# Performance work log

Measured on AMD Instinct MI355X. Metric: run time of the kernel, lower is better.

Reference implementation:

```python
import math
import jax, jax.numpy as jnp
import numpy as np

B, S, D = 4, 2048, 1280
H, HD = 16, 80  # num_heads, head_dim
LOG2E = 1.442695041


def setup_inputs() -> dict:
    key = jax.random.key(0)
    ks = jax.random.split(key, 6)
    hidden_states = jax.random.normal(ks[0], (B, S, D), dtype=jnp.float32)
    # additive causal mask: 0 on/below diagonal, large negative above
    causal = jnp.tril(jnp.ones((S, S), dtype=bool))
    attention_mask = jnp.where(causal, 0.0, -1e9).astype(jnp.float32)[None, None, :, :]
    attention_mask = jnp.broadcast_to(attention_mask, (B, 1, S, S))
    scaling = jax.random.normal(ks[1], (HD,), dtype=jnp.float32)
    fan = 1.0 / math.sqrt(D)
    qkv_w = jax.random.normal(ks[2], (3 * H * HD, D), dtype=jnp.float32) * fan
    qkv_b = jax.random.normal(ks[3], (3 * H * HD,), dtype=jnp.float32) * fan
    o_w = jax.random.normal(ks[4], (D, H * HD), dtype=jnp.float32) * (1.0 / math.sqrt(H * HD))
    o_b = jax.random.normal(ks[5], (D,), dtype=jnp.float32) * fan
    return {
        "hidden_states": hidden_states,
        "attention_mask": attention_mask,
        "scaling": scaling,
        "qkv_w": qkv_w,
        "qkv_b": qkv_b,
        "o_w": o_w,
        "o_b": o_b,
    }


def reference(hidden_states, attention_mask, scaling, qkv_w, qkv_b, o_w, o_b):
    b, s, _ = hidden_states.shape
    qkv = hidden_states @ qkv_w.T + qkv_b  # [b, s, 3*H*HD]
    xq, xk, xv = jnp.split(qkv, [H * HD, 2 * H * HD], axis=-1)
    xq = xq.reshape(b, s, H, HD)
    xk = xk.reshape(b, s, H, HD)
    xv = xv.reshape(b, s, H, HD)
    # per-dim query scaling: softplus(scaling) * log2(e) / sqrt(head_dim)
    scale = jax.nn.softplus(scaling) * (LOG2E / math.sqrt(HD))
    xq = xq * scale[None, None, None, :]
    scores = jnp.einsum("bqhd,bkhd->bhqk", xq, xk) + attention_mask  # [b,H,s,s]
    probs = jax.nn.softmax(scores.astype(jnp.float32), axis=-1).astype(xq.dtype)
    out = jnp.einsum("bhqk,bkhd->bqhd", probs, xv).reshape(b, s, H * HD)
    return out @ o_w.T + o_b
```

## Files before the change

kernel.cpp:

```cpp
#include <hip/hip_runtime.h>
#include <math.h>

#define B_ 4
#define S_ 2048
#define D_ 1280
#define H_ 16
#define HD_ 80
#define HHD (H_ * HD_)
#define QKVN (3 * H_ * HD_)

typedef __bf16 bf16x8 __attribute__((ext_vector_type(8)));
typedef __bf16 bf16x4 __attribute__((ext_vector_type(4)));
typedef float  f32x4  __attribute__((ext_vector_type(4)));

__global__ __launch_bounds__(256) void cvt_bf16(
    const float* __restrict__ in, __bf16* __restrict__ out, int n8)
{
    const int i = blockIdx.x * 256 + threadIdx.x;
    if (i < n8) {
        const float4 a = ((const float4*)in)[2 * (size_t)i];
        const float4 b = ((const float4*)in)[2 * (size_t)i + 1];
        bf16x8 v = {(__bf16)a.x, (__bf16)a.y, (__bf16)a.z, (__bf16)a.w,
                    (__bf16)b.x, (__bf16)b.y, (__bf16)b.z, (__bf16)b.w};
        *(bf16x8*)(out + 8 * (size_t)i) = v;
    }
}

__device__ __forceinline__ void async_copy16(const void* g, void* l)
{
    __builtin_amdgcn_global_load_lds(
        (const __attribute__((address_space(1))) unsigned int*)g,
        (__attribute__((address_space(3))) unsigned int*)l, 16, 0, 0);
}

__device__ __forceinline__ void stage128x64(
    const __bf16* __restrict__ src, int K, char* lds, int tid)
{
    const int wave = tid >> 6, lane = tid & 63;
#pragma unroll
    for (int i = 0; i < 4; ++i) {
        const int c = (wave * 4 + i) * 64 + lane;
        const int r = c >> 3;
        const int g = (c & 7) ^ (r & 7);
        async_copy16(src + (size_t)r * K + g * 8, lds + (wave * 4 + i) * 1024);
    }
}

__device__ __forceinline__ bf16x8 frag_ld(const char* lds, int m, int j)
{
    return *(const bf16x8*)(lds + m * 128 + ((j ^ (m & 7)) << 4));
}

__device__ __forceinline__ void mfma_loop(
    const __bf16* __restrict__ A, const __bf16* __restrict__ W, int K,
    char* ldsA, char* ldsB, int tid, f32x4 acc[4][4])
{
    const int wave = tid >> 6;
    const int wm = wave >> 1, wn = wave & 1;
    const int l16 = tid & 15, quad = (tid & 63) >> 4;

#pragma unroll
    for (int mi = 0; mi < 4; ++mi)
#pragma unroll
        for (int ni = 0; ni < 4; ++ni) acc[mi][ni] = (f32x4){0.f, 0.f, 0.f, 0.f};

    for (int k0 = 0; k0 < K; k0 += 64) {
        __syncthreads();
        stage128x64(A + k0, K, ldsA, tid);
        stage128x64(W + k0, K, ldsB, tid);
        __syncthreads();
#pragma unroll
        for (int ks = 0; ks < 2; ++ks) {
            bf16x8 af[4], bfr[4];
#pragma unroll
            for (int mi = 0; mi < 4; ++mi)
                af[mi] = frag_ld(ldsA, wm * 64 + mi * 16 + l16, ks * 4 + quad);
#pragma unroll
            for (int ni = 0; ni < 4; ++ni)
                bfr[ni] = frag_ld(ldsB, wn * 64 + ni * 16 + l16, ks * 4 + quad);
#pragma unroll
            for (int mi = 0; mi < 4; ++mi)
#pragma unroll
                for (int ni = 0; ni < 4; ++ni)
                    acc[mi][ni] = __builtin_amdgcn_mfma_f32_16x16x32_bf16(
                        af[mi], bfr[ni], acc[mi][ni], 0, 0, 0);
        }
    }
}

__global__ __launch_bounds__(256) void gemm_qkv_mfma(
    const __bf16* __restrict__ Ab, const __bf16* __restrict__ Wb,
    const float* __restrict__ bias, const float* __restrict__ scaling,
    __bf16* __restrict__ Qb, __bf16* __restrict__ Kb, __bf16* __restrict__ Vtb)
{
    __shared__ __align__(16) char ldsA[128 * 128];
    __shared__ __align__(16) char ldsB[128 * 128];
    const int tid = threadIdx.x;
    const int m0 = blockIdx.y * 128, n0 = blockIdx.x * 128;

    f32x4 acc[4][4];
    mfma_loop(Ab + (size_t)m0 * D_, Wb + (size_t)n0 * D_, D_, ldsA, ldsB, tid, acc);

    const int wave = tid >> 6, wm = wave >> 1, wn = wave & 1;
    const int l16 = tid & 15, quad = (tid & 63) >> 4;
    const int sec = n0 / HHD;

#pragma unroll
    for (int ni = 0; ni < 4; ++ni) {
        const int col = n0 + wn * 64 + ni * 16 + l16;
        const int cis = col - sec * HHD;
        const int h = cis / HD_;
        const int d = cis - h * HD_;
        const float bv = bias[col];
        float qsv = 0.f;
        if (sec == 0)
            qsv = log1pf(expf(scaling[d])) *
                  (1.442695041f * 1.442695041f / 8.944271910f);
#pragma unroll
        for (int mi = 0; mi < 4; ++mi) {
#pragma unroll
            for (int r = 0; r < 4; ++r) {
                const int row = m0 + wm * 64 + mi * 16 + quad * 4 + r;
                const int bb = row >> 11;
                const int s = row & (S_ - 1);
                const size_t bh = (size_t)(bb * H_ + h);
                const float v = acc[mi][ni][r] + bv;
                if (sec == 0)      Qb[(bh * S_ + s) * HD_ + d] = (__bf16)(v * qsv);
                else if (sec == 1) Kb[(bh * S_ + s) * HD_ + d] = (__bf16)v;
                else               Vtb[(bh * HD_ + d) * S_ + s] = (__bf16)v;
            }
        }
    }
}

__global__ __launch_bounds__(256) void gemm_o_mfma(
    const __bf16* __restrict__ Ab, const __bf16* __restrict__ Wb,
    const float* __restrict__ bias, float* __restrict__ C)
{
    __shared__ __align__(16) char ldsA[128 * 128];
    __shared__ __align__(16) char ldsB[128 * 128];
    const int tid = threadIdx.x;
    const int m0 = blockIdx.y * 128, n0 = blockIdx.x * 128;

    f32x4 acc[4][4];
    mfma_loop(Ab + (size_t)m0 * D_, Wb + (size_t)n0 * D_, D_, ldsA, ldsB, tid, acc);

    const int wave = tid >> 6, wm = wave >> 1, wn = wave & 1;
    const int l16 = tid & 15, quad = (tid & 63) >> 4;

#pragma unroll
    for (int ni = 0; ni < 4; ++ni) {
        const int col = n0 + wn * 64 + ni * 16 + l16;
        const float bv = bias[col];
#pragma unroll
        for (int mi = 0; mi < 4; ++mi) {
#pragma unroll
            for (int r = 0; r < 4; ++r) {
                const int row = m0 + wm * 64 + mi * 16 + quad * 4 + r;
                C[(size_t)row * D_ + col] = acc[mi][ni][r] + bv;
            }
        }
    }
}

__global__ __launch_bounds__(256, 4) void attn_v7(
    const __bf16* __restrict__ Qb, const __bf16* __restrict__ Kb,
    const __bf16* __restrict__ Vtb, __bf16* __restrict__ out)
{
    __shared__ __align__(16) __bf16 Ps[4][2][16][40];

    const int tid = threadIdx.x;
    const int wave = tid >> 6;
    const int lane = tid & 63;
    const int l16 = lane & 15;
    const int quad = lane >> 4;
    const int b = blockIdx.z, h = blockIdx.y;
    const int bh = b * H_ + h;
    const int x = blockIdx.x;
    const int q_lo = 64 * x + 16 * wave;
    const int q_hi = 64 * (31 - x) + 16 * wave;

    const __bf16* Kbase = Kb + (size_t)bh * S_ * HD_;
    const __bf16* Vbase = Vtb + (size_t)bh * HD_ * S_;

    bf16x8 qfL[3], qfH[3];
    {
        const __bf16* QrowL = Qb + ((size_t)bh * S_ + q_lo + l16) * HD_;
        const __bf16* QrowH = Qb + ((size_t)bh * S_ + q_hi + l16) * HD_;
        qfL[0] = *(const bf16x8*)(QrowL + quad * 8);
        qfL[1] = *(const bf16x8*)(QrowL + 32 + quad * 8);
        qfH[0] = *(const bf16x8*)(QrowH + quad * 8);
        qfH[1] = *(const bf16x8*)(QrowH + 32 + quad * 8);
        bf16x8 zL = {}, zH = {};
        if (quad < 2) {
            zL = *(const bf16x8*)(QrowL + 64 + quad * 8);
            zH = *(const bf16x8*)(QrowH + 64 + quad * 8);
        }
        qfL[2] = zL; qfH[2] = zH;
    }

    float mL = -1e30f, lL = 0.f, mH = -1e30f, lH = 0.f;
    f32x4 oL[5], oH[5];
#pragma unroll
    for (int t = 0; t < 5; ++t) { oL[t] = (f32x4){0.f,0.f,0.f,0.f}; oH[t] = (f32x4){0.f,0.f,0.f,0.f}; }

    const int nkt_lo = (q_lo + 16 + 31) >> 5;
    const int nkt_hi = (q_hi + 16 + 31) >> 5;

    for (int kt = 0; kt < nkt_hi; ++kt) {
        const int k0 = kt * 32;
        const bool do_lo = (kt < nkt_lo);

        f32x4 sH[2], sL[2];
#pragma unroll
        for (int t = 0; t < 2; ++t) {
            const __bf16* Krow = Kbase + (size_t)(k0 + t * 16 + l16) * HD_;
            const bf16x8 kf0 = *(const bf16x8*)(Krow + quad * 8);
            const bf16x8 kf1 = *(const bf16x8*)(Krow + 32 + quad * 8);
            bf16x8 kf2 = {};
            if (quad < 2) kf2 = *(const bf16x8*)(Krow + 64 + quad * 8);

            f32x4 a = (f32x4){0.f,0.f,0.f,0.f};
            a = __builtin_amdgcn_mfma_f32_16x16x32_bf16(kf0, qfH[0], a, 0, 0, 0);
            a = __builtin_amdgcn_mfma_f32_16x16x32_bf16(kf1, qfH[1], a, 0, 0, 0);
            a = __builtin_amdgcn_mfma_f32_16x16x32_bf16(kf2, qfH[2], a, 0, 0, 0);
            sH[t] = a;
            if (do_lo) {
                f32x4 c = (f32x4){0.f,0.f,0.f,0.f};
                c = __builtin_amdgcn_mfma_f32_16x16x32_bf16(kf0, qfL[0], c, 0, 0, 0);
                c = __builtin_amdgcn_mfma_f32_16x16x32_bf16(kf1, qfL[1], c, 0, 0, 0);
                c = __builtin_amdgcn_mfma_f32_16x16x32_bf16(kf2, qfL[2], c, 0, 0, 0);
                sL[t] = c;
            }
        }

        float aH;
        {
            if (k0 + 31 > q_hi) {
#pragma unroll
                for (int t = 0; t < 2; ++t)
#pragma unroll
                    for (int i = 0; i < 4; ++i)
                        sH[t][i] = (k0 + t * 16 + quad * 4 + i <= q_hi + l16)
                                   ? sH[t][i] : -1e30f;
            }
            float mx = sH[0][0];
#pragma unroll
            for (int i = 1; i < 4; ++i) mx = fmaxf(mx, sH[0][i]);
#pragma unroll
            for (int i = 0; i < 4; ++i) mx = fmaxf(mx, sH[1][i]);
            mx = fmaxf(mx, __shfl_xor(mx, 16));
            mx = fmaxf(mx, __shfl_xor(mx, 32));
            const float mn = fmaxf(mH, mx);
            aH = exp2f(mH - mn);
            mH = mn;
            float rs = 0.f;
#pragma unroll
            for (int t = 0; t < 2; ++t)
#pragma unroll
                for (int i = 0; i < 4; ++i) {
                    const float p = exp2f(sH[t][i] - mn);
                    sH[t][i] = p;
                    rs += p;
                }
            rs += __shfl_xor(rs, 16);
            rs += __shfl_xor(rs, 32);
            lH = lH * aH + rs;
#pragma unroll
            for (int t = 0; t < 2; ++t) {
                bf16x4 pk = {(__bf16)sH[t][0], (__bf16)sH[t][1],
                             (__bf16)sH[t][2], (__bf16)sH[t][3]};
                *(bf16x4*)&Ps[wave][0][l16][t * 16 + quad * 4] = pk;
            }
        }

        float aL = 1.f;
        if (do_lo) {
            if (k0 + 31 > q_lo) {
#pragma unroll
                for (int t = 0; t < 2; ++t)
#pragma unroll
                    for (int i = 0; i < 4; ++i)
                        sL[t][i] = (k0 + t * 16 + quad * 4 + i <= q_lo + l16)
                                   ? sL[t][i] : -1e30f;
            }
            float mx = sL[0][0];
#pragma unroll
            for (int i = 1; i < 4; ++i) mx = fmaxf(mx, sL[0][i]);
#pragma unroll
            for (int i = 0; i < 4; ++i) mx = fmaxf(mx, sL[1][i]);
            mx = fmaxf(mx, __shfl_xor(mx, 16));
            mx = fmaxf(mx, __shfl_xor(mx, 32));
            const float mn = fmaxf(mL, mx);
            aL = exp2f(mL - mn);
            mL = mn;
            float rs = 0.f;
#pragma unroll
            for (int t = 0; t < 2; ++t)
#pragma unroll
                for (int i = 0; i < 4; ++i) {
                    const float p = exp2f(sL[t][i] - mn);
                    sL[t][i] = p;
                    rs += p;
                }
            rs += __shfl_xor(rs, 16);
            rs += __shfl_xor(rs, 32);
            lL = lL * aL + rs;
#pragma unroll
            for (int t = 0; t < 2; ++t) {
                bf16x4 pk = {(__bf16)sL[t][0], (__bf16)sL[t][1],
                             (__bf16)sL[t][2], (__bf16)sL[t][3]};
                *(bf16x4*)&Ps[wave][1][l16][t * 16 + quad * 4] = pk;
            }
        }

        bf16x8 vf[5];
#pragma unroll
        for (int t = 0; t < 5; ++t)
            vf[t] = *(const bf16x8*)(Vbase + (size_t)(t * 16 + l16) * S_ + k0 + quad * 8);

        asm volatile("s_waitcnt lgkmcnt(0)" ::: "memory");
        const bf16x8 pfH = *(const bf16x8*)&Ps[wave][0][l16][quad * 8];
        const bf16x8 pfL = *(const bf16x8*)&Ps[wave][1][l16][quad * 8];

#pragma unroll
        for (int t = 0; t < 5; ++t) {
            f32x4 c;
#pragma unroll
            for (int i = 0; i < 4; ++i) c[i] = oH[t][i] * aH;
            oH[t] = __builtin_amdgcn_mfma_f32_16x16x32_bf16(vf[t], pfH, c, 0, 0, 0);
            if (do_lo) {
                f32x4 d;
#pragma unroll
                for (int i = 0; i < 4; ++i) d[i] = oL[t][i] * aL;
                oL[t] = __builtin_amdgcn_mfma_f32_16x16x32_bf16(vf[t], pfL, d, 0, 0, 0);
            }
        }
    }

    const float invH = 1.f / lH;
    const float invL = 1.f / lL;
    const size_t rowH = ((size_t)b * S_ + q_hi + l16) * HHD + h * HD_ + quad * 4;
    const size_t rowL = ((size_t)b * S_ + q_lo + l16) * HHD + h * HD_ + quad * 4;
#pragma unroll
    for (int t = 0; t < 5; ++t) {
        bf16x4 ovH = {(__bf16)(oH[t][0] * invH), (__bf16)(oH[t][1] * invH),
                      (__bf16)(oH[t][2] * invH), (__bf16)(oH[t][3] * invH)};
        bf16x4 ovL = {(__bf16)(oL[t][0] * invL), (__bf16)(oL[t][1] * invL),
                      (__bf16)(oL[t][2] * invL), (__bf16)(oL[t][3] * invL)};
        *(bf16x4*)(out + rowH + t * 16) = ovH;
        *(bf16x4*)(out + rowL + t * 16) = ovL;
    }
}

extern "C" void kernel_launch(void* const* d_in, const int* in_sizes, int n_in,
                              void* d_out, int out_size, void* d_ws, size_t ws_size,
                              hipStream_t stream)
{
    const float* hidden  = (const float*)d_in[0];
    const float* scaling = (const float*)d_in[2];
    const float* qkv_w   = (const float*)d_in[3];
    const float* qkv_b   = (const float*)d_in[4];
    const float* o_w     = (const float*)d_in[5];
    const float* o_b     = (const float*)d_in[6];
    float* out = (float*)d_out;

    const size_t N_HID = (size_t)B_ * S_ * D_;
    const size_t N_QW  = (size_t)QKVN * D_;
    const size_t N_OW  = (size_t)D_ * D_;
    const size_t NPH   = (size_t)B_ * H_ * S_ * HD_;

    __bf16* Ab    = (__bf16*)d_ws;
    __bf16* Wqb   = Ab + N_HID;
    __bf16* Wob   = Wqb + N_QW;
    __bf16* Qb    = Wob + N_OW;
    __bf16* Kb    = Qb + NPH;
    __bf16* Vtb   = Kb + NPH;
    __bf16* attnb = Vtb + NPH;

    dim3 blk(256);

    cvt_bf16<<<dim3(N_HID / 8 / 256), blk, 0, stream>>>(hidden, Ab, N_HID / 8);
    cvt_bf16<<<dim3(N_QW  / 8 / 256), blk, 0, stream>>>(qkv_w, Wqb, N_QW / 8);
    cvt_bf16<<<dim3(N_OW  / 8 / 256), blk, 0, stream>>>(o_w,   Wob, N_OW / 8);

    gemm_qkv_mfma<<<dim3(QKVN / 128, B_ * S_ / 128), blk, 0, stream>>>(
        Ab, Wqb, qkv_b, scaling, Qb, Kb, Vtb);

    attn_v7<<<dim3(16, H_, B_), blk, 0, stream>>>(Qb, Kb, Vtb, attnb);

    gemm_o_mfma<<<dim3(D_ / 128, B_ * S_ / 128), blk, 0, stream>>>(
        attnb, Wob, o_b, out);
}
```

Before: 539.7 us.

## Double-buffer K fragments, remap attention grid, and defer row-sum reduction

The attention kernel now prefetches the next K tile into registers while the current tile is processed, using a ping-pong pair of register buffers. The V loads are issued at the top of each iteration so their global latency overlaps with the QK MFMAs, and s_setprio raises wave priority around the MFMA blocks. The row-sum shuffle reduction is moved out of the loop and done once at the end, which is valid because the per-lane partial sums share the same rescale factors. The grid is flattened and remapped so that 8 consecutive blocks come from different heads with the same x, which changes L2 locality and load balance. The cost is higher register pressure at 4 waves/SIMD occupancy.

After: 1.006 ms. 1.86x slower.

```diff
diff --git a/kernel.cpp b/kernel.cpp
--- a/kernel.cpp
+++ b/kernel.cpp
@@ -163,7 +163,20 @@
     }
 }
 
-__global__ __launch_bounds__(256, 4) void attn_v7(
+struct KF8 { bf16x8 f0, f1, f2; };
+
+__device__ __forceinline__ void kload8(
+    const __bf16* __restrict__ base, int row, int quad, KF8& kf)
+{
+    const __bf16* r = base + (size_t)row * HD_;
+    kf.f0 = *(const bf16x8*)(r + quad * 8);
+    kf.f1 = *(const bf16x8*)(r + 32 + quad * 8);
+    bf16x8 z = {};
+    if (quad < 2) z = *(const bf16x8*)(r + 64 + quad * 8);
+    kf.f2 = z;
+}
+
+__global__ __launch_bounds__(256, 4) void attn_v9(
     const __bf16* __restrict__ Qb, const __bf16* __restrict__ Kb,
     const __bf16* __restrict__ Vtb, __bf16* __restrict__ out)
 {
@@ -174,30 +187,23 @@
     const int lane = tid & 63;
     const int l16 = lane & 15;
     const int quad = lane >> 4;
-    const int b = blockIdx.z, h = blockIdx.y;
-    const int bh = b * H_ + h;
-    const int x = blockIdx.x;
+
+    const int flat = blockIdx.x;
+    const int slot = flat >> 3;
+    const int bh   = ((slot >> 4) << 3) + (flat & 7);
+    const int x    = slot & 15;
+    const int b = bh >> 4, h = bh & 15;
+
     const int q_lo = 64 * x + 16 * wave;
     const int q_hi = 64 * (31 - x) + 16 * wave;
 
+    const __bf16* Qbase = Qb + (size_t)bh * S_ * HD_;
     const __bf16* Kbase = Kb + (size_t)bh * S_ * HD_;
     const __bf16* Vbase = Vtb + (size_t)bh * HD_ * S_;
 
-    bf16x8 qfL[3], qfH[3];
-    {
-        const __bf16* QrowL = Qb + ((size_t)bh * S_ + q_lo + l16) * HD_;
-        const __bf16* QrowH = Qb + ((size_t)bh * S_ + q_hi + l16) * HD_;
-        qfL[0] = *(const bf16x8*)(QrowL + quad * 8);
-        qfL[1] = *(const bf16x8*)(QrowL + 32 + quad * 8);
-        qfH[0] = *(const bf16x8*)(QrowH + quad * 8);
-        qfH[1] = *(const bf16x8*)(QrowH + 32 + quad * 8);
-        bf16x8 zL = {}, zH = {};
-        if (quad < 2) {
-            zL = *(const bf16x8*)(QrowL + 64 + quad * 8);
-            zH = *(const bf16x8*)(QrowH + 64 + quad * 8);
-        }
-        qfL[2] = zL; qfH[2] = zH;
-    }
+    KF8 qL, qH;
+    kload8(Qbase, q_lo + l16, quad, qL);
+    kload8(Qbase, q_hi + l16, quad, qH);
 
     float mL = -1e30f, lL = 0.f, mH = -1e30f, lH = 0.f;
     f32x4 oL[5], oH[5];
@@ -207,31 +213,42 @@
     const int nkt_lo = (q_lo + 16 + 31) >> 5;
     const int nkt_hi = (q_hi + 16 + 31) >> 5;
 
-    for (int kt = 0; kt < nkt_hi; ++kt) {
+    KF8 kA[2], kB[2];
+    kload8(Kbase, l16, quad, kA[0]);
+    kload8(Kbase, 16 + l16, quad, kA[1]);
+
+    auto body = [&](int kt, KF8 (&cur)[2], KF8 (&nxt)[2]) {
         const int k0 = kt * 32;
         const bool do_lo = (kt < nkt_lo);
 
+        bf16x8 vf[5];
+#pragma unroll
+        for (int t = 0; t < 5; ++t)
+            vf[t] = *(const bf16x8*)(Vbase + (size_t)(t * 16 + l16) * S_ + k0 + quad * 8);
+
         f32x4 sH[2], sL[2];
+        __builtin_amdgcn_s_setprio(1);
 #pragma unroll
         for (int t = 0; t < 2; ++t) {
-            const __bf16* Krow = Kbase + (size_t)(k0 + t * 16 + l16) * HD_;
-            const bf16x8 kf0 = *(const bf16x8*)(Krow + quad * 8);
-            const bf16x8 kf1 = *(const bf16x8*)(Krow + 32 + quad * 8);
-            bf16x8 kf2 = {};
-            if (quad < 2) kf2 = *(const bf16x8*)(Krow + 64 + quad * 8);
-
             f32x4 a = (f32x4){0.f,0.f,0.f,0.f};
-            a = __builtin_amdgcn_mfma_f32_16x16x32_bf16(kf0, qfH[0], a, 0, 0, 0);
-            a = __builtin_amdgcn_mfma_f32_16x16x32_bf16(kf1, qfH[1], a, 0, 0, 0);
-            a = __builtin_amdgcn_mfma_f32_16x16x32_bf16(kf2, qfH[2], a, 0, 0, 0);
+            a = __builtin_amdgcn_mfma_f32_16x16x32_bf16(cur[t].f0, qH.f0, a, 0, 0, 0);
+            a = __builtin_amdgcn_mfma_f32_16x16x32_bf16(cur[t].f1, qH.f1, a, 0, 0, 0);
+            a = __builtin_amdgcn_mfma_f32_16x16x32_bf16(cur[t].f2, qH.f2, a, 0, 0, 0);
             sH[t] = a;
             if (do_lo) {
                 f32x4 c = (f32x4){0.f,0.f,0.f,0.f};
-                c = __builtin_amdgcn_mfma_f32_16x16x32_bf16(kf0, qfL[0], c, 0, 0, 0);
-                c = __builtin_amdgcn_mfma_f32_16x16x32_bf16(kf1, qfL[1], c, 0, 0, 0);
-                c = __builtin_amdgcn_mfma_f32_16x16x32_bf16(kf2, qfL[2], c, 0, 0, 0);
+                c = __builtin_amdgcn_mfma_f32_16x16x32_bf16(cur[t].f0, qL.f0, c, 0, 0, 0);
+                c = __builtin_amdgcn_mfma_f32_16x16x32_bf16(cur[t].f1, qL.f1, c, 0, 0, 0);
+                c = __builtin_amdgcn_mfma_f32_16x16x32_bf16(cur[t].f2, qL.f2, c, 0, 0, 0);
                 sL[t] = c;
             }
+        }
+        __builtin_amdgcn_s_setprio(0);
+
+        {
+            const int kn = (kt + 1 < nkt_hi ? kt + 1 : kt) * 32;
+            kload8(Kbase, kn + l16, quad, nxt[0]);
+            kload8(Kbase, kn + 16 + l16, quad, nxt[1]);
         }
 
         float aH;
@@ -244,11 +261,11 @@
                         sH[t][i] = (k0 + t * 16 + quad * 4 + i <= q_hi + l16)
                                    ? sH[t][i] : -1e30f;
             }
-            float mx = sH[0][0];
-#pragma unroll
-            for (int i = 1; i < 4; ++i) mx = fmaxf(mx, sH[0][i]);
-#pragma unroll
-            for (int i = 0; i < 4; ++i) mx = fmaxf(mx, sH[1][i]);
+            float m01 = fmaxf(sH[0][0], sH[0][1]);
+            float m23 = fmaxf(sH[0][2], sH[0][3]);
+            float m45 = fmaxf(sH[1][0], sH[1][1]);
+            float m67 = fmaxf(sH[1][2], sH[1][3]);
+            float mx = fmaxf(fmaxf(m01, m23), fmaxf(m45, m67));
             mx = fmaxf(mx, __shfl_xor(mx, 16));
             mx = fmaxf(mx, __shfl_xor(mx, 32));
             const float mn = fmaxf(mH, mx);
@@ -263,8 +280,6 @@
                     sH[t][i] = p;
                     rs += p;
                 }
-            rs += __shfl_xor(rs, 16);
-            rs += __shfl_xor(rs, 32);
             lH = lH * aH + rs;
 #pragma unroll
             for (int t = 0; t < 2; ++t) {
@@ -284,11 +299,11 @@
                         sL[t][i] = (k0 + t * 16 + quad * 4 + i <= q_lo + l16)
                                    ? sL[t][i] : -1e30f;
             }
-            float mx = sL[0][0];
-#pragma unroll
-            for (int i = 1; i < 4; ++i) mx = fmaxf(mx, sL[0][i]);
-#pragma unroll
-            for (int i = 0; i < 4; ++i) mx = fmaxf(mx, sL[1][i]);
+            float m01 = fmaxf(sL[0][0], sL[0][1]);
+            float m23 = fmaxf(sL[0][2], sL[0][3]);
+            float m45 = fmaxf(sL[1][0], sL[1][1]);
+            float m67 = fmaxf(sL[1][2], sL[1][3]);
+            float mx = fmaxf(fmaxf(m01, m23), fmaxf(m45, m67));
             mx = fmaxf(mx, __shfl_xor(mx, 16));
             mx = fmaxf(mx, __shfl_xor(mx, 32));
             const float mn = fmaxf(mL, mx);
@@ -303,8 +318,6 @@
                     sL[t][i] = p;
                     rs += p;
                 }
-            rs += __shfl_xor(rs, 16);
-            rs += __shfl_xor(rs, 32);
             lL = lL * aL + rs;
 #pragma unroll
             for (int t = 0; t < 2; ++t) {
@@ -314,15 +327,11 @@
             }
         }
 
-        bf16x8 vf[5];
-#pragma unroll
-        for (int t = 0; t < 5; ++t)
-            vf[t] = *(const bf16x8*)(Vbase + (size_t)(t * 16 + l16) * S_ + k0 + quad * 8);
-
         asm volatile("s_waitcnt lgkmcnt(0)" ::: "memory");
         const bf16x8 pfH = *(const bf16x8*)&Ps[wave][0][l16][quad * 8];
         const bf16x8 pfL = *(const bf16x8*)&Ps[wave][1][l16][quad * 8];
 
+        __builtin_amdgcn_s_setprio(1);
 #pragma unroll
         for (int t = 0; t < 5; ++t) {
             f32x4 c;
@@ -336,10 +345,23 @@
                 oL[t] = __builtin_amdgcn_mfma_f32_16x16x32_bf16(vf[t], pfL, d, 0, 0, 0);
             }
         }
-    }
-
-    const float invH = 1.f / lH;
-    const float invL = 1.f / lL;
+        __builtin_amdgcn_s_setprio(0);
+    };
+
+    int kt = 0;
+    while (true) {
+        body(kt, kA, kB);
+        if (++kt == nkt_hi) break;
+        body(kt, kB, kA);
+        if (++kt == nkt_hi) break;
+    }
+
+    float lHs = lH + __shfl_xor(lH, 16);
+    lHs += __shfl_xor(lHs, 32);
+    float lLs = lL + __shfl_xor(lL, 16);
+    lLs += __shfl_xor(lLs, 32);
+    const float invH = 1.f / lHs;
+    const float invL = 1.f / lLs;
     const size_t rowH = ((size_t)b * S_ + q_hi + l16) * HHD + h * HD_ + quad * 4;
     const size_t rowL = ((size_t)b * S_ + q_lo + l16) * HHD + h * HD_ + quad * 4;
 #pragma unroll
@@ -387,7 +409,7 @@
     gemm_qkv_mfma<<<dim3(QKVN / 128, B_ * S_ / 128), blk, 0, stream>>>(
         Ab, Wqb, qkv_b, scaling, Qb, Kb, Vtb);
 
-    attn_v7<<<dim3(16, H_, B_), blk, 0, stream>>>(Qb, Kb, Vtb, attnb);
+    attn_v9<<<dim3(16 * H_ * B_), blk, 0, stream>>>(Qb, Kb, Vtb, attnb);
 
     gemm_o_mfma<<<dim3(D_ / 128, B_ * S_ / 128), blk, 0, stream>>>(
         attnb, Wob, o_b, out);
```
